# Kernel tuning notes

Measured on AMD Instinct MI355X. Metric: run time of the kernel, lower is better.

Reference implementation:

```python
import jax, jax.numpy as jnp
import numpy as np

N = 100000   # nodes
E = 640000   # edges
DIN = 128
DOUT = 128
BN_EPS = 1e-5


def setup_inputs() -> dict:
    key = jax.random.key(0)
    k = jax.random.split(key, 6)
    x = jax.random.normal(k[0], (N, DIN), dtype=jnp.float32)
    edge_index = jax.random.randint(k[1], (2, E), 0, N, dtype=jnp.int64)
    # MLP params: Linear(DIN,DOUT) -> BatchNorm1d(DOUT) -> ReLU -> Linear(DOUT,DOUT)
    s1 = 1.0 / np.sqrt(DIN)
    s2 = 1.0 / np.sqrt(DOUT)
    W1 = jax.random.uniform(k[2], (DIN, DOUT), jnp.float32, -s1, s1)
    b1 = jax.random.uniform(k[3], (DOUT,), jnp.float32, -s1, s1)
    gamma = jnp.ones((DOUT,), jnp.float32)
    beta = jnp.zeros((DOUT,), jnp.float32)
    W2 = jax.random.uniform(k[4], (DOUT, DOUT), jnp.float32, -s2, s2)
    b2 = jax.random.uniform(k[5], (DOUT,), jnp.float32, -s2, s2)
    eps = jnp.zeros((), jnp.float32)  # train_eps=True, init 0.0
    return {"x": x, "edge_index": edge_index, "W1": W1, "b1": b1,
            "gamma": gamma, "beta": beta, "W2": W2, "b2": b2, "eps": eps}


def reference(x, edge_index, W1, b1, gamma, beta, W2, b2, eps):
    src = edge_index[0]
    dst = edge_index[1]
    # GIN sum aggregation: gather source features, scatter-add to target nodes
    agg = jax.ops.segment_sum(x[src], dst, num_segments=N)  # [N, DIN]
    h = agg + (1.0 + eps) * x  # eps-weighted residual combine
    # MLP: Linear -> BatchNorm1d (training stats, biased var) -> ReLU -> Linear
    h = h @ W1 + b1  # [N, DOUT]
    mu = jnp.mean(h, axis=0)
    var = jnp.mean((h - mu) ** 2, axis=0)
    h = (h - mu) * jax.lax.rsqrt(var + BN_EPS) * gamma + beta
    h = jnp.maximum(h, 0.0)
    return h @ W2 + b2
```

## Files before the change

kernel.cpp:

```cpp
#include <hip/hip_runtime.h>

#define N_NODES 100000
#define DIM     128
#define NEDGE   640000
#define BN_EPS  1e-5f
#define NB_SCAN 98

#define PB_CNT  2500
#define PB_X    6250
#define PB_W    64

#define NBUCKET 64
#define T_TILES 4
#define GGRID   1563
#define AGRID   6250

typedef __bf16 bf16x8 __attribute__((ext_vector_type(8)));
typedef float  f32x4  __attribute__((ext_vector_type(4)));
typedef unsigned short u16x8 __attribute__((ext_vector_type(8)));

__device__ __forceinline__ unsigned short f2b(float f) {
    unsigned u = __builtin_bit_cast(unsigned, f);
    u += 0x7fffu + ((u >> 16) & 1u);
    return (unsigned short)(u >> 16);
}
__device__ __forceinline__ float b2f(unsigned short b) {
    return __builtin_bit_cast(float, ((unsigned)b) << 16);
}

__global__ __launch_bounds__(256) void k_prep(const float* __restrict__ x,
                                              const float* __restrict__ W1,
                                              const float* __restrict__ W2,
                                              const int* __restrict__ ei,
                                              unsigned short* __restrict__ xb,
                                              unsigned short* __restrict__ Wt1,
                                              unsigned short* __restrict__ Wt2,
                                              int* __restrict__ rowptr,
                                              unsigned short* __restrict__ rank) {
    const int b = blockIdx.x;
    const int t = threadIdx.x;
    if (b < PB_CNT) {
        int e = b * 256 + t;
        int r = atomicAdd(&rowptr[ei[NEDGE + e]], 1);
        rank[e] = (unsigned short)r;
    } else if (b < PB_CNT + PB_X) {
        size_t base = ((size_t)(b - PB_CNT) * 256 + t) * 8;
        float4 v0 = *(const float4*)(x + base);
        float4 v1 = *(const float4*)(x + base + 4);
        u16x8 o;
        o[0] = f2b(v0.x); o[1] = f2b(v0.y); o[2] = f2b(v0.z); o[3] = f2b(v0.w);
        o[4] = f2b(v1.x); o[5] = f2b(v1.y); o[6] = f2b(v1.z); o[7] = f2b(v1.w);
        *(u16x8*)(xb + base) = o;
    } else if (b < PB_CNT + PB_X + PB_W) {
        int idx = (b - PB_CNT - PB_X) * 256 + t;
        int k = idx >> 7, n = idx & 127;
        Wt1[n * 128 + k] = f2b(W1[idx]);
    } else {
        int idx = (b - PB_CNT - PB_X - PB_W) * 256 + t;
        int k = idx >> 7, n = idx & 127;
        Wt2[n * 128 + k] = f2b(W2[idx]);
    }
}

__global__ __launch_bounds__(256) void k_scan1(int* __restrict__ rowptr,
                                               int* __restrict__ bsum) {
    __shared__ int tsum[256];
    const int t = threadIdx.x;
    const int base = blockIdx.x * 1024 + t * 4;
    int v[4];
    #pragma unroll
    for (int j = 0; j < 4; ++j)
        v[j] = (base + j < N_NODES) ? rowptr[base + j] : 0;
    int s = v[0] + v[1] + v[2] + v[3];
    tsum[t] = s;
    __syncthreads();
    #pragma unroll
    for (int off = 1; off < 256; off <<= 1) {
        int a = tsum[t];
        int b = (t >= off) ? tsum[t - off] : 0;
        __syncthreads();
        tsum[t] = a + b;
        __syncthreads();
    }
    int run = tsum[t] - s;
    #pragma unroll
    for (int j = 0; j < 4; ++j) {
        int nv = run;
        run += v[j];
        if (base + j < N_NODES) rowptr[base + j] = nv;
    }
    if (t == 255) bsum[blockIdx.x] = tsum[255];
}

__global__ __launch_bounds__(256) void k_scan_add(int* __restrict__ rowptr,
                                                  const int* __restrict__ bsum) {
    __shared__ int sh[128];
    const int t = threadIdx.x;
    if (t < 128) sh[t] = (t < NB_SCAN) ? bsum[t] : 0;
    __syncthreads();
    #pragma unroll
    for (int off = 1; off < 128; off <<= 1) {
        int a = 0, b = 0;
        if (t < 128) { a = sh[t]; b = (t >= off) ? sh[t - off] : 0; }
        __syncthreads();
        if (t < 128) sh[t] = a + b;
        __syncthreads();
    }
    const int add = (blockIdx.x > 0) ? sh[blockIdx.x - 1] : 0;
    const int base = blockIdx.x * 1024 + t * 4;
    #pragma unroll
    for (int j = 0; j < 4; ++j) {
        if (base + j < N_NODES) rowptr[base + j] += add;
    }
    if (blockIdx.x == 0 && t == 0) rowptr[N_NODES] = NEDGE;
}

__global__ __launch_bounds__(256) void k_fill(const int* __restrict__ ei,
                                              const int* __restrict__ rowptr,
                                              const unsigned short* __restrict__ rank,
                                              int* __restrict__ srcidx) {
    int e = blockIdx.x * 256 + threadIdx.x;
    if (e < NEDGE) {
        int dst = ei[NEDGE + e];
        srcidx[rowptr[dst] + (int)rank[e]] = ei[e];
    }
}

__global__ __launch_bounds__(256) void k_agg1(const unsigned short* __restrict__ xb,
                                              const int* __restrict__ rowptr,
                                              const int* __restrict__ srcidx,
                                              const float* __restrict__ epsp,
                                              const unsigned short* __restrict__ Wt,
                                              const float* __restrict__ b1,
                                              unsigned short* __restrict__ hB,
                                              float* __restrict__ buckets) {
    __shared__ __align__(16) unsigned short At[16 * 136];
    __shared__ __align__(16) unsigned short stage[4][512];
    const int t = threadIdx.x;
    const int w = t >> 6;
    const int lane = t & 63;
    const int n15 = lane & 15;
    const int quad = lane >> 4;
    const int c8 = n15 * 8;

    const int row0 = blockIdx.x * 16;
    const int node = row0 + w * 4 + quad;

    int4 Bfr[2][4];
    const unsigned short* wp = Wt + (w * 32 + n15) * 128 + quad * 8;
    #pragma unroll
    for (int c = 0; c < 2; ++c)
        #pragma unroll
        for (int ks = 0; ks < 4; ++ks)
            Bfr[c][ks] = *(const int4*)(wp + c * 16 * 128 + ks * 32);
    float bias[2] = { b1[w * 32 + n15], b1[w * 32 + 16 + n15] };
    const float scale = 1.0f + epsp[0];

    const int beg = rowptr[node];
    const int end = rowptr[node + 1];
    float acc[8];
    {
        u16x8 v = *(const u16x8*)(xb + (size_t)node * 128 + c8);
        #pragma unroll
        for (int j = 0; j < 8; ++j) acc[j] = scale * b2f(v[j]);
    }
    for (int p = beg; p < end; p += 4) {
        const int np = end - p;
        int i0 = srcidx[p];
        int i1 = (np > 1) ? srcidx[p + 1] : i0;
        int i2 = (np > 2) ? srcidx[p + 2] : i0;
        int i3 = (np > 3) ? srcidx[p + 3] : i0;
        u16x8 v0 = *(const u16x8*)(xb + (size_t)i0 * 128 + c8);
        u16x8 v1 = *(const u16x8*)(xb + (size_t)i1 * 128 + c8);
        u16x8 v2 = *(const u16x8*)(xb + (size_t)i2 * 128 + c8);
        u16x8 v3 = *(const u16x8*)(xb + (size_t)i3 * 128 + c8);
        #pragma unroll
        for (int j = 0; j < 8; ++j) acc[j] += b2f(v0[j]);
        if (np > 1) {
            #pragma unroll
            for (int j = 0; j < 8; ++j) acc[j] += b2f(v1[j]);
        }
        if (np > 2) {
            #pragma unroll
            for (int j = 0; j < 8; ++j) acc[j] += b2f(v2[j]);
        }
        if (np > 3) {
            #pragma unroll
            for (int j = 0; j < 8; ++j) acc[j] += b2f(v3[j]);
        }
    }
    {
        u16x8 o;
        #pragma unroll
        for (int j = 0; j < 8; ++j) o[j] = f2b(acc[j]);
        *(u16x8*)(At + (w * 4 + quad) * 136 + c8) = o;
    }
    __syncthreads();

    f32x4 accm[2] = {};
    #pragma unroll
    for (int ks = 0; ks < 4; ++ks) {
        int4 araw = *(const int4*)(At + n15 * 136 + ks * 32 + quad * 8);
        bf16x8 af = __builtin_bit_cast(bf16x8, araw);
        #pragma unroll
        for (int c = 0; c < 2; ++c)
            accm[c] = __builtin_amdgcn_mfma_f32_16x16x32_bf16(
                af, __builtin_bit_cast(bf16x8, Bfr[c][ks]), accm[c], 0, 0, 0);
    }
    float s[2] = {0.f, 0.f}, q[2] = {0.f, 0.f};
    unsigned short* st = stage[w];
    #pragma unroll
    for (int c = 0; c < 2; ++c)
        #pragma unroll
        for (int r = 0; r < 4; ++r) {
            float v = accm[c][r] + bias[c];
            s[c] += v; q[c] += v * v;
            st[(quad * 4 + r) * 32 + c * 16 + n15] = f2b(v);
        }
    {
        int so = lane * 8;
        int r = so >> 5, cc = so & 31;
        *(int4*)(hB + (size_t)(row0 + r) * 128 + w * 32 + cc) = *(const int4*)(st + so);
    }

    #pragma unroll
    for (int c = 0; c < 2; ++c) {
        s[c] += __shfl_down(s[c], 32); q[c] += __shfl_down(q[c], 32);
        s[c] += __shfl_down(s[c], 16); q[c] += __shfl_down(q[c], 16);
    }
    if (quad == 0) {
        float* bk = buckets + (blockIdx.x & (NBUCKET - 1)) * 256;
        atomicAdd(&bk[w * 32 + n15], s[0]);
        atomicAdd(&bk[w * 32 + 16 + n15], s[1]);
        atomicAdd(&bk[128 + w * 32 + n15], q[0]);
        atomicAdd(&bk[128 + w * 32 + 16 + n15], q[1]);
    }
}

__global__ void k_finalize(const float* __restrict__ gamma,
                           const float* __restrict__ beta,
                           const float* __restrict__ buckets,
                           float* __restrict__ aff) {
    int c = threadIdx.x;
    if (c < DIM) {
        float s = 0.f, q = 0.f;
        #pragma unroll 8
        for (int b = 0; b < NBUCKET; ++b) {
            s += buckets[b * 256 + c];
            q += buckets[b * 256 + 128 + c];
        }
        float mu  = s * (1.0f / N_NODES);
        float var = q * (1.0f / N_NODES) - mu * mu;
        float a = gamma[c] * rsqrtf(var + BN_EPS);
        aff[c] = a;
        aff[DIM + c] = beta[c] - mu * a;
    }
}

__global__ __launch_bounds__(256) void k_gemm2(const unsigned short* __restrict__ hb,
                                               const unsigned short* __restrict__ Wt2,
                                               const float* __restrict__ aff,
                                               const float* __restrict__ b2,
                                               float* __restrict__ out) {
    __shared__ __align__(16) unsigned short Asb[2][16 * 136];
    __shared__ __align__(16) float stage[4][512];
    const int t = threadIdx.x;
    const int w = t >> 6;
    const int lane = t & 63;
    const int n15 = lane & 15;
    const int quad = lane >> 4;
    const int kb = w * 32 + quad * 8;

    int4 Bfr[2][4];
    const unsigned short* wp = Wt2 + (w * 32 + n15) * 128 + quad * 8;
    #pragma unroll
    for (int c = 0; c < 2; ++c)
        #pragma unroll
        for (int ks = 0; ks < 4; ++ks)
            Bfr[c][ks] = *(const int4*)(wp + c * 16 * 128 + ks * 32);

    float akr[8], bkr[8];
    *(float4*)(akr)     = *(const float4*)(aff + kb);
    *(float4*)(akr + 4) = *(const float4*)(aff + kb + 4);
    *(float4*)(bkr)     = *(const float4*)(aff + 128 + kb);
    *(float4*)(bkr + 4) = *(const float4*)(aff + 128 + kb + 4);
    float bias[2] = { b2[w * 32 + n15], b2[w * 32 + 16 + n15] };

    const int tile0 = blockIdx.x * T_TILES;
    int4 gr;
    {
        int r0 = tile0 * 16;
        if (r0 < N_NODES)
            gr = *(const int4*)(hb + (size_t)(r0 + n15) * 128 + kb);
    }
    float* st = stage[w];

    #pragma unroll
    for (int i = 0; i < T_TILES; ++i) {
        const int row0 = (tile0 + i) * 16;
        const bool valid = row0 < N_NODES;
        unsigned short* al = Asb[i & 1];
        if (valid) {
            u16x8 ar = __builtin_bit_cast(u16x8, gr);
            u16x8 pr;
            #pragma unroll
            for (int j = 0; j < 8; ++j)
                pr[j] = f2b(fmaxf(fmaf(b2f(ar[j]), akr[j], bkr[j]), 0.f));
            *(int4*)(al + n15 * 136 + kb) = __builtin_bit_cast(int4, pr);
        }
        if (i + 1 < T_TILES) {
            int rn = (tile0 + i + 1) * 16;
            if (rn < N_NODES)
                gr = *(const int4*)(hb + (size_t)(rn + n15) * 128 + kb);
        }
        __syncthreads();
        if (valid) {
            f32x4 acc[2] = {};
            #pragma unroll
            for (int ks = 0; ks < 4; ++ks) {
                int4 araw = *(const int4*)(al + n15 * 136 + ks * 32 + quad * 8);
                bf16x8 af = __builtin_bit_cast(bf16x8, araw);
                #pragma unroll
                for (int c = 0; c < 2; ++c)
                    acc[c] = __builtin_amdgcn_mfma_f32_16x16x32_bf16(
                        af, __builtin_bit_cast(bf16x8, Bfr[c][ks]), acc[c], 0, 0, 0);
            }
            #pragma unroll
            for (int c = 0; c < 2; ++c)
                #pragma unroll
                for (int r = 0; r < 4; ++r)
                    st[(quad * 4 + r) * 32 + c * 16 + n15] = acc[c][r] + bias[c];
            #pragma unroll
            for (int p = 0; p < 2; ++p) {
                int fo = p * 256 + lane * 4;
                int r = fo >> 5, cc = fo & 31;
                *(float4*)(out + (size_t)(row0 + r) * 128 + w * 32 + cc) =
                    *(const float4*)(st + fo);
            }
        }
    }
}

extern "C" void kernel_launch(void* const* d_in, const int* in_sizes, int n_in,
                              void* d_out, int out_size, void* d_ws, size_t ws_size,
                              hipStream_t stream) {
    const float* x     = (const float*)d_in[0];
    const int*   ei    = (const int*)d_in[1];
    const float* W1    = (const float*)d_in[2];
    const float* b1    = (const float*)d_in[3];
    const float* gamma = (const float*)d_in[4];
    const float* beta  = (const float*)d_in[5];
    const float* W2    = (const float*)d_in[6];
    const float* b2    = (const float*)d_in[7];
    const float* eps   = (const float*)d_in[8];
    float* out = (float*)d_out;

    float* buckets      = (float*)d_ws;
    int* rowptr         = (int*)(buckets + NBUCKET * 256);
    float* aff          = (float*)(rowptr + N_NODES + 4);
    unsigned short* hB  = (unsigned short*)(aff + 256);
    unsigned short* xb  = hB + (size_t)N_NODES * DIM;
    unsigned short* Wt1 = xb + (size_t)N_NODES * DIM;
    unsigned short* Wt2 = Wt1 + 16384;
    int* srcidx         = (int*)(Wt2 + 16384);
    int* bsum           = srcidx + NEDGE;
    unsigned short* rank = hB;

    hipMemsetAsync(buckets, 0,
                   NBUCKET * 256 * sizeof(float) + (N_NODES + 4) * sizeof(int), stream);

    k_prep<<<PB_CNT + PB_X + 2 * PB_W, 256, 0, stream>>>(x, W1, W2, ei, xb, Wt1, Wt2,
                                                         rowptr, rank);
    k_scan1<<<NB_SCAN, 256, 0, stream>>>(rowptr, bsum);
    k_scan_add<<<NB_SCAN, 256, 0, stream>>>(rowptr, bsum);
    k_fill<<<(NEDGE + 255) / 256, 256, 0, stream>>>(ei, rowptr, rank, srcidx);
    k_agg1<<<AGRID, 256, 0, stream>>>(xb, rowptr, srcidx, eps, Wt1, b1, hB, buckets);
    k_finalize<<<1, 128, 0, stream>>>(gamma, beta, buckets, aff);
    k_gemm2<<<GGRID, 256, 0, stream>>>(hB, Wt2, aff, b2, out);
}
```

Baseline: 229.8 us.

## Replicate degree counters and batch neighbor gathers with shuffled indices

Degree counting now atomically increments one of four replicated counter arrays, selected by block, to spread atomic contention. The scan folds the replicas into per-replica offsets that the fill kernel uses to place each edge. The aggregation loop now loads up to 16 neighbor indices cooperatively per lane group, broadcasts them with shuffles, and issues 8 row gathers back-to-back to raise memory-level parallelism. The cost is extra counter memory and traffic, plus some wasted loads on low-degree nodes.

Measured after the change: 222.0 us. 3.4% less time.

```diff
diff --git a/kernel.cpp b/kernel.cpp
--- a/kernel.cpp
+++ b/kernel.cpp
@@ -10,6 +10,7 @@
 #define PB_X    6250
 #define PB_W    64
 
+#define RREP    4
 #define NBUCKET 64
 #define T_TILES 4
 #define GGRID   1563
@@ -35,14 +36,16 @@
                                               unsigned short* __restrict__ xb,
                                               unsigned short* __restrict__ Wt1,
                                               unsigned short* __restrict__ Wt2,
-                                              int* __restrict__ rowptr,
+                                              int* __restrict__ cnt,
                                               unsigned short* __restrict__ rank) {
     const int b = blockIdx.x;
     const int t = threadIdx.x;
     if (b < PB_CNT) {
         int e = b * 256 + t;
-        int r = atomicAdd(&rowptr[ei[NEDGE + e]], 1);
-        rank[e] = (unsigned short)r;
+        int dst = ei[NEDGE + e];
+        int r = b & (RREP - 1);
+        int rk = atomicAdd(&cnt[(size_t)r * N_NODES + dst], 1);
+        rank[e] = (unsigned short)rk;
     } else if (b < PB_CNT + PB_X) {
         size_t base = ((size_t)(b - PB_CNT) * 256 + t) * 8;
         float4 v0 = *(const float4*)(x + base);
@@ -62,15 +65,29 @@
     }
 }
 
-__global__ __launch_bounds__(256) void k_scan1(int* __restrict__ rowptr,
+__global__ __launch_bounds__(256) void k_scan1(int* __restrict__ cnt,
+                                               int* __restrict__ rowptr,
                                                int* __restrict__ bsum) {
     __shared__ int tsum[256];
     const int t = threadIdx.x;
     const int base = blockIdx.x * 1024 + t * 4;
-    int v[4];
-    #pragma unroll
-    for (int j = 0; j < 4; ++j)
-        v[j] = (base + j < N_NODES) ? rowptr[base + j] : 0;
+    int v[4] = {0, 0, 0, 0};
+    if (base < N_NODES) {
+        int4 c0 = *(const int4*)(cnt + base);
+        int4 c1 = *(const int4*)(cnt + N_NODES + base);
+        int4 c2 = *(const int4*)(cnt + 2 * N_NODES + base);
+        int4 c3 = *(const int4*)(cnt + 3 * N_NODES + base);
+        int4 z  = {0, 0, 0, 0};
+        int4 s01, s012;
+        s01.x = c0.x + c1.x; s01.y = c0.y + c1.y; s01.z = c0.z + c1.z; s01.w = c0.w + c1.w;
+        s012.x = s01.x + c2.x; s012.y = s01.y + c2.y; s012.z = s01.z + c2.z; s012.w = s01.w + c2.w;
+        *(int4*)(cnt + base) = z;
+        *(int4*)(cnt + N_NODES + base) = c0;
+        *(int4*)(cnt + 2 * N_NODES + base) = s01;
+        *(int4*)(cnt + 3 * N_NODES + base) = s012;
+        v[0] = s012.x + c3.x; v[1] = s012.y + c3.y;
+        v[2] = s012.z + c3.z; v[3] = s012.w + c3.w;
+    }
     int s = v[0] + v[1] + v[2] + v[3];
     tsum[t] = s;
     __syncthreads();
@@ -93,6 +110,7 @@
 }
 
 __global__ __launch_bounds__(256) void k_scan_add(int* __restrict__ rowptr,
+                                                  int* __restrict__ cnt,
                                                   const int* __restrict__ bsum) {
     __shared__ int sh[128];
     const int t = threadIdx.x;
@@ -108,21 +126,29 @@
     }
     const int add = (blockIdx.x > 0) ? sh[blockIdx.x - 1] : 0;
     const int base = blockIdx.x * 1024 + t * 4;
-    #pragma unroll
-    for (int j = 0; j < 4; ++j) {
-        if (base + j < N_NODES) rowptr[base + j] += add;
+    if (base < N_NODES) {
+        int4 rp = *(const int4*)(rowptr + base);
+        rp.x += add; rp.y += add; rp.z += add; rp.w += add;
+        *(int4*)(rowptr + base) = rp;
+        #pragma unroll
+        for (int r = 0; r < RREP; ++r) {
+            int4 cp = *(const int4*)(cnt + r * N_NODES + base);
+            cp.x += rp.x; cp.y += rp.y; cp.z += rp.z; cp.w += rp.w;
+            *(int4*)(cnt + r * N_NODES + base) = cp;
+        }
     }
     if (blockIdx.x == 0 && t == 0) rowptr[N_NODES] = NEDGE;
 }
 
 __global__ __launch_bounds__(256) void k_fill(const int* __restrict__ ei,
-                                              const int* __restrict__ rowptr,
+                                              const int* __restrict__ cnt,
                                               const unsigned short* __restrict__ rank,
                                               int* __restrict__ srcidx) {
     int e = blockIdx.x * 256 + threadIdx.x;
     if (e < NEDGE) {
         int dst = ei[NEDGE + e];
-        srcidx[rowptr[dst] + (int)rank[e]] = ei[e];
+        int r = (e >> 8) & (RREP - 1);
+        srcidx[cnt[(size_t)r * N_NODES + dst] + (int)rank[e]] = ei[e];
     }
 }
 
@@ -142,6 +168,7 @@
     const int n15 = lane & 15;
     const int quad = lane >> 4;
     const int c8 = n15 * 8;
+    const int gbase = lane & 48;
 
     const int row0 = blockIdx.x * 16;
     const int node = row0 + w * 4 + quad;
@@ -164,29 +191,39 @@
         #pragma unroll
         for (int j = 0; j < 8; ++j) acc[j] = scale * b2f(v[j]);
     }
-    for (int p = beg; p < end; p += 4) {
-        const int np = end - p;
-        int i0 = srcidx[p];
-        int i1 = (np > 1) ? srcidx[p + 1] : i0;
-        int i2 = (np > 2) ? srcidx[p + 2] : i0;
-        int i3 = (np > 3) ? srcidx[p + 3] : i0;
-        u16x8 v0 = *(const u16x8*)(xb + (size_t)i0 * 128 + c8);
-        u16x8 v1 = *(const u16x8*)(xb + (size_t)i1 * 128 + c8);
-        u16x8 v2 = *(const u16x8*)(xb + (size_t)i2 * 128 + c8);
-        u16x8 v3 = *(const u16x8*)(xb + (size_t)i3 * 128 + c8);
-        #pragma unroll
-        for (int j = 0; j < 8; ++j) acc[j] += b2f(v0[j]);
-        if (np > 1) {
-            #pragma unroll
-            for (int j = 0; j < 8; ++j) acc[j] += b2f(v1[j]);
-        }
-        if (np > 2) {
-            #pragma unroll
-            for (int j = 0; j < 8; ++j) acc[j] += b2f(v2[j]);
-        }
-        if (np > 3) {
-            #pragma unroll
-            for (int j = 0; j < 8; ++j) acc[j] += b2f(v3[j]);
+    for (int p = beg; p < end; p += 16) {
+        const int m = end - p;
+        int li = (n15 < m) ? n15 : (m - 1);
+        int myi = srcidx[p + li];
+        int4 va[8];
+        #pragma unroll
+        for (int k = 0; k < 8; ++k) {
+            int ik = __shfl(myi, gbase + k);
+            va[k] = *(const int4*)(xb + (size_t)ik * 128 + c8);
+        }
+        #pragma unroll
+        for (int k = 0; k < 8; ++k) {
+            if (k < m) {
+                u16x8 v = __builtin_bit_cast(u16x8, va[k]);
+                #pragma unroll
+                for (int j = 0; j < 8; ++j) acc[j] += b2f(v[j]);
+            }
+        }
+        if (m > 8) {
+            int4 vb[8];
+            #pragma unroll
+            for (int k = 0; k < 8; ++k) {
+                int ik = __shfl(myi, gbase + 8 + k);
+                vb[k] = *(const int4*)(xb + (size_t)ik * 128 + c8);
+            }
+            #pragma unroll
+            for (int k = 0; k < 8; ++k) {
+                if (k + 8 < m) {
+                    u16x8 v = __builtin_bit_cast(u16x8, vb[k]);
+                    #pragma unroll
+                    for (int j = 0; j < 8; ++j) acc[j] += b2f(v[j]);
+                }
+            }
         }
     }
     {
@@ -356,7 +393,8 @@
     float* out = (float*)d_out;
 
     float* buckets      = (float*)d_ws;
-    int* rowptr         = (int*)(buckets + NBUCKET * 256);
+    int* cnt            = (int*)(buckets + NBUCKET * 256);
+    int* rowptr         = cnt + RREP * N_NODES;
     float* aff          = (float*)(rowptr + N_NODES + 4);
     unsigned short* hB  = (unsigned short*)(aff + 256);
     unsigned short* xb  = hB + (size_t)N_NODES * DIM;
@@ -367,13 +405,13 @@
     unsigned short* rank = hB;
 
     hipMemsetAsync(buckets, 0,
-                   NBUCKET * 256 * sizeof(float) + (N_NODES + 4) * sizeof(int), stream);
+                   NBUCKET * 256 * sizeof(float) + RREP * N_NODES * sizeof(int), stream);
 
     k_prep<<<PB_CNT + PB_X + 2 * PB_W, 256, 0, stream>>>(x, W1, W2, ei, xb, Wt1, Wt2,
-                                                         rowptr, rank);
-    k_scan1<<<NB_SCAN, 256, 0, stream>>>(rowptr, bsum);
-    k_scan_add<<<NB_SCAN, 256, 0, stream>>>(rowptr, bsum);
-    k_fill<<<(NEDGE + 255) / 256, 256, 0, stream>>>(ei, rowptr, rank, srcidx);
+                                                         cnt, rank);
+    k_scan1<<<NB_SCAN, 256, 0, stream>>>(cnt, rowptr, bsum);
+    k_scan_add<<<NB_SCAN, 256, 0, stream>>>(rowptr, cnt, bsum);
+    k_fill<<<(NEDGE + 255) / 256, 256, 0, stream>>>(ei, cnt, rank, srcidx);
     k_agg1<<<AGRID, 256, 0, stream>>>(xb, rowptr, srcidx, eps, Wt1, b1, hB, buckets);
     k_finalize<<<1, 128, 0, stream>>>(gamma, beta, buckets, aff);
     k_gemm2<<<GGRID, 256, 0, stream>>>(hB, Wt2, aff, b2, out);
```
